# Kernel optimization log

Hardware: AMD Instinct MI355X
Metric: run time of the kernel (lower is better)

Reference implementation:

```python
import jax, jax.numpy as jnp
import numpy as np

B, H, W, D, K = 64, 32, 32, 128, 1024


def setup_inputs() -> dict:
    key = jax.random.key(0)
    k1, k2 = jax.random.split(key)
    z_e = jax.random.normal(k1, (B, H, W, D), dtype=jnp.float32)
    # GlorotUniform over (k, d): limit = sqrt(6 / (k + d))
    limit = float(np.sqrt(6.0 / (K + D)))
    codebook = jax.random.uniform(k2, (K, D), dtype=jnp.float32, minval=-limit, maxval=limit)
    return {"z_e": z_e, "codebook": codebook}


def reference(z_e, codebook):
    # Original: norm = ||z_e[..., None, :] - codebook||_2 over d, then argmin over k.
    # Squared distance has the same argmin; expand to avoid the (B,H,W,k,d) tensor:
    # ||z - c||^2 = ||z||^2 - 2 z.c + ||c||^2
    z2 = jnp.sum(z_e * z_e, axis=-1, keepdims=True)           # (B,H,W,1)
    c2 = jnp.sum(codebook * codebook, axis=-1)                # (k,)
    dots = jnp.einsum('bhwd,kd->bhwk', z_e, codebook)         # (B,H,W,k)
    dist2 = z2 - 2.0 * dots + c2                              # (B,H,W,k)
    q_z = jnp.argmin(dist2, axis=-1)                          # (B,H,W) int
    return q_z
```

## Files before the change

kernel.cpp:

```cpp
#include <hip/hip_runtime.h>
#include <stdint.h>

#define NPTS   65536
#define DDIM   128
#define KCODES 1024

typedef __attribute__((ext_vector_type(8))) _Float16  half8;
typedef __attribute__((ext_vector_type(4))) float     f32x4;
typedef __attribute__((ext_vector_type(4))) int       int4v;
typedef __attribute__((ext_vector_type(2))) _Float16  half2v;

__device__ __forceinline__ void split16(float x, _Float16& hi, _Float16& lo) {
  _Float16 h = (__builtin_fabsf(x) < 6.103515625e-05f) ? (_Float16)0.f : (_Float16)x;
  hi = h;
  lo = (_Float16)(__fmul_rn(__fsub_rn(x, (float)h), 2048.f));
}

__device__ __forceinline__ float np_sumsq_128(const float* __restrict__ row) {
  float r[8];
#pragma unroll
  for (int k = 0; k < 8; ++k) r[k] = __fmul_rn(row[k], row[k]);
  for (int i = 8; i < 128; i += 8)
#pragma unroll
    for (int k = 0; k < 8; ++k) r[k] = __fadd_rn(r[k], __fmul_rn(row[i + k], row[i + k]));
  float s01 = __fadd_rn(r[0], r[1]), s23 = __fadd_rn(r[2], r[3]);
  float s45 = __fadd_rn(r[4], r[5]), s67 = __fadd_rn(r[6], r[7]);
  return __fadd_rn(__fadd_rn(s01, s23), __fadd_rn(s45, s67));
}

__device__ __forceinline__ void async_copy16(const void* g, void* l) {
  auto gp = (const __attribute__((address_space(1))) unsigned int*)(uintptr_t)g;
  auto lp = (__attribute__((address_space(3))) unsigned int*)(unsigned)(uintptr_t)l;
  __builtin_amdgcn_global_load_lds(gp, lp, 16, 0, 0);
}

constexpr size_t SZ_B   = (size_t)KCODES * DDIM * 2;
constexpr size_t OFF_B1 = 0;
constexpr size_t OFF_B2 = SZ_B;
constexpr size_t OFF_C2 = 2 * SZ_B;
constexpr size_t WS_NEED = OFF_C2 + (size_t)KCODES * 4;

__global__ __launch_bounds__(256) void vq_prep_cb(const float* __restrict__ cb,
                                                  _Float16* __restrict__ B1,
                                                  _Float16* __restrict__ B2,
                                                  float* __restrict__ c2) {
  const int w = threadIdx.x >> 6, ln = threadIdx.x & 63;
  const int code = blockIdx.x * 4 + w;
  const float2 cv = ((const float2*)(cb + (size_t)code * DDIM))[ln];
  _Float16 h0, l0, h1, l1;
  split16(cv.x, h0, l0); split16(cv.y, h1, l1);
  const int kg = ln >> 2;
  const int o  = 2 * (ln & 3);
  const size_t dst = (size_t)code * DDIM + (size_t)((kg ^ (code & 15)) * 8 + o);
  *(half2v*)(B1 + dst) = (half2v){h0, h1};
  *(half2v*)(B2 + dst) = (half2v){l0, l1};

  if (threadIdx.x < 32) {
    const int cc = blockIdx.x * 4 + (threadIdx.x >> 3), jj = threadIdx.x & 7;
    const float* row = cb + (size_t)cc * DDIM;
    float e = row[jj];
    float acc = __fmul_rn(e, e);
    for (int i = 1; i < 16; ++i) {
      e = row[i * 8 + jj];
      acc = __fadd_rn(acc, __fmul_rn(e, e));
    }
    float a1 = __fadd_rn(acc, __shfl_xor(acc, 1));
    float a2 = __fadd_rn(a1, __shfl_xor(a1, 2));
    float a4 = __fadd_rn(a2, __shfl_xor(a2, 4));
    if (jj == 0) c2[cc] = a4;
  }
}

__global__ __launch_bounds__(256, 2) void vq_gemm(
    const float* __restrict__ z,
    const unsigned short* __restrict__ B1g, const unsigned short* __restrict__ B2g,
    const float* __restrict__ c2g, int* __restrict__ out) {
  __shared__ alignas(16) char smem[16384 + 16384 + 4096 + 512];
  unsigned short* Bs1 = (unsigned short*)smem;
  unsigned short* Bs2 = (unsigned short*)(smem + 16384);
  float* c2sh = (float*)(smem + 32768);
  float* z2sh = (float*)(smem + 32768 + 4096);
  float* Ls   = (float*)smem;

  const int tid = threadIdx.x;
  const int ln = tid & 63, wr = tid >> 6;
  const int l15 = ln & 15, q = ln >> 4;
  const size_t row0 = (size_t)blockIdx.x * 128;
  const float4* z4 = (const float4*)z;

  for (int cc = 0; cc < 4; ++cc) {
#pragma unroll
    for (int j = 0; j < 4; ++j) {
      const int idx = tid + j * 256;
      float4 v = z4[(row0 + cc * 32) * 32 + idx];
      *(float4*)&Ls[(idx >> 5) * 132 + (idx & 31) * 4] = v;
    }
    __syncthreads();
    {
      const int r = tid >> 3, jj = tid & 7;
      const float* row = &Ls[r * 132];
      float e = row[jj];
      float acc = __fmul_rn(e, e);
      for (int i = 1; i < 16; ++i) {
        e = row[i * 8 + jj];
        acc = __fadd_rn(acc, __fmul_rn(e, e));
      }
      float a1 = __fadd_rn(acc, __shfl_xor(acc, 1));
      float a2 = __fadd_rn(a1, __shfl_xor(a1, 2));
      float a4 = __fadd_rn(a2, __shfl_xor(a2, 4));
      if (jj == 0) z2sh[cc * 32 + r] = a4;
    }
    __syncthreads();
  }

#pragma unroll
  for (int j = 0; j < 4; ++j) {
    const int s = tid + j * 256;
    async_copy16(B2g + s * 8, Bs2 + s * 8);
    async_copy16(B1g + s * 8, Bs1 + s * 8);
  }
  async_copy16(c2g + tid * 4, c2sh + tid * 4);

  half8 a1f[2][4], a2f[2][4];
#pragma unroll
  for (int rf = 0; rf < 2; ++rf) {
    const float* zr = z + (row0 + wr * 32 + rf * 16 + l15) * DDIM;
#pragma unroll
    for (int ks = 0; ks < 4; ++ks) {
      float tmp[8];
      *(float4*)tmp       = *(const float4*)(zr + ks * 32 + q * 8);
      *(float4*)(tmp + 4) = *(const float4*)(zr + ks * 32 + q * 8 + 4);
      half8 h, l;
#pragma unroll
      for (int e = 0; e < 8; ++e) {
        _Float16 hh, ll;
        split16(tmp[e], hh, ll);
        h[e] = hh; l[e] = ll;
      }
      a1f[rf][ks] = h; a2f[rf][ks] = l;
    }
  }

  float mv[8];
  int mi[8];
#pragma unroll
  for (int i = 0; i < 8; ++i) { mv[i] = 3.0e38f; mi[i] = 0; }

  __syncthreads();

  float z2r[8];
#pragma unroll
  for (int rf = 0; rf < 2; ++rf)
#pragma unroll
    for (int reg = 0; reg < 4; ++reg)
      z2r[rf * 4 + reg] = z2sh[wr * 32 + rf * 16 + q * 4 + reg];

  for (int iter = 0; iter < 16; ++iter) {
    const int c0 = iter * 64;
    f32x4 acc[2][4];
#pragma unroll
    for (int rf = 0; rf < 2; ++rf)
#pragma unroll
      for (int cf = 0; cf < 4; ++cf) acc[rf][cf] = (f32x4){0.f, 0.f, 0.f, 0.f};

#pragma unroll
    for (int ks = 0; ks < 4; ++ks) {
      half8 b[4];
#pragma unroll
      for (int cf = 0; cf < 4; ++cf)
        b[cf] = *(const half8*)&Bs2[(cf * 16 + l15) * 128 + (((ks * 4 + q) ^ l15) * 8)];
#pragma unroll
      for (int rf = 0; rf < 2; ++rf)
#pragma unroll
        for (int cf = 0; cf < 4; ++cf)
          acc[rf][cf] = __builtin_amdgcn_mfma_f32_16x16x32_f16(a1f[rf][ks], b[cf],
                                                               acc[rf][cf], 0, 0, 0);
    }

    __syncthreads();
    if (iter < 15) {
#pragma unroll
      for (int j = 0; j < 4; ++j) {
        const int s = tid + j * 256;
        async_copy16(B2g + (size_t)(c0 + 64) * DDIM + s * 8, Bs2 + s * 8);
      }
    }

#pragma unroll
    for (int ks = 0; ks < 4; ++ks) {
      half8 b[4];
#pragma unroll
      for (int cf = 0; cf < 4; ++cf)
        b[cf] = *(const half8*)&Bs1[(cf * 16 + l15) * 128 + (((ks * 4 + q) ^ l15) * 8)];
#pragma unroll
      for (int rf = 0; rf < 2; ++rf)
#pragma unroll
        for (int cf = 0; cf < 4; ++cf)
          acc[rf][cf] = __builtin_amdgcn_mfma_f32_16x16x32_f16(a2f[rf][ks], b[cf],
                                                               acc[rf][cf], 0, 0, 0);
    }
#pragma unroll
    for (int rf = 0; rf < 2; ++rf)
#pragma unroll
      for (int cf = 0; cf < 4; ++cf) acc[rf][cf] = acc[rf][cf] * 4.8828125e-4f;

#pragma unroll
    for (int ks = 0; ks < 4; ++ks) {
      half8 b[4];
#pragma unroll
      for (int cf = 0; cf < 4; ++cf)
        b[cf] = *(const half8*)&Bs1[(cf * 16 + l15) * 128 + (((ks * 4 + q) ^ l15) * 8)];
#pragma unroll
      for (int rf = 0; rf < 2; ++rf)
#pragma unroll
        for (int cf = 0; cf < 4; ++cf)
          acc[rf][cf] = __builtin_amdgcn_mfma_f32_16x16x32_f16(a1f[rf][ks], b[cf],
                                                               acc[rf][cf], 0, 0, 0);
    }

#pragma unroll
    for (int rf = 0; rf < 2; ++rf)
#pragma unroll
      for (int reg = 0; reg < 4; ++reg) {
        const int slot = rf * 4 + reg;
        const float z2v = z2r[slot];
#pragma unroll
        for (int cf = 0; cf < 4; ++cf) {
          const float c2v = c2sh[c0 + cf * 16 + l15];
          float dot = acc[rf][cf][reg];
          float v = __fadd_rn(__fsub_rn(z2v, __fmul_rn(2.f, dot)), c2v);
          int idx = c0 + cf * 16 + l15;
          if (v < mv[slot]) { mv[slot] = v; mi[slot] = idx; }
        }
      }

    __syncthreads();
    if (iter < 15) {
#pragma unroll
      for (int j = 0; j < 4; ++j) {
        const int s = tid + j * 256;
        async_copy16(B1g + (size_t)(c0 + 64) * DDIM + s * 8, Bs1 + s * 8);
      }
    }
  }

#pragma unroll
  for (int slot = 0; slot < 8; ++slot) {
    float v = mv[slot];
    int i = mi[slot];
#pragma unroll
    for (int m = 1; m <= 8; m <<= 1) {
      float ov = __shfl_xor(v, m);
      int oi = __shfl_xor(i, m);
      if (ov < v || (ov == v && oi < i)) { v = ov; i = oi; }
    }
    mv[slot] = v; mi[slot] = i;
  }

  if (l15 == 0) {
#pragma unroll
    for (int rf = 0; rf < 2; ++rf) {
      int4v r = {mi[rf * 4 + 0], mi[rf * 4 + 1], mi[rf * 4 + 2], mi[rf * 4 + 3]};
      *(int4v*)&out[row0 + wr * 32 + rf * 16 + q * 4] = r;
    }
  }
}

__global__ __launch_bounds__(256) void vq_fallback(const float* __restrict__ z,
                                                   const float* __restrict__ cb,
                                                   int* __restrict__ out) {
  __shared__ float zs[DDIM];
  __shared__ float z2s;
  __shared__ float bv[256];
  __shared__ int bi[256];
  const int p = blockIdx.x, tid = threadIdx.x;
  if (tid < DDIM) zs[tid] = z[(size_t)p * DDIM + tid];
  __syncthreads();
  if (tid == 0) z2s = np_sumsq_128(zs);
  __syncthreads();
  const float z2p = z2s;
  float best = 3.0e38f;
  int bidx = 0;
  for (int c = tid; c < KCODES; c += 256) {
    const float* cr = cb + (size_t)c * DDIM;
    double acc = 0.0;
#pragma unroll 8
    for (int d = 0; d < DDIM; ++d) acc += (double)zs[d] * (double)cr[d];
    float dfl = (float)acc;
    float c2k = np_sumsq_128(cr);
    float v = __fadd_rn(__fsub_rn(z2p, __fmul_rn(2.f, dfl)), c2k);
    if (v < best) { best = v; bidx = c; }
  }
  bv[tid] = best; bi[tid] = bidx;
  __syncthreads();
  for (int off = 128; off > 0; off >>= 1) {
    if (tid < off) {
      if (bv[tid + off] < bv[tid] || (bv[tid + off] == bv[tid] && bi[tid + off] < bi[tid])) {
        bv[tid] = bv[tid + off]; bi[tid] = bi[tid + off];
      }
    }
    __syncthreads();
  }
  if (tid == 0) out[p] = bi[0];
}

extern "C" void kernel_launch(void* const* d_in, const int* in_sizes, int n_in,
                              void* d_out, int out_size, void* d_ws, size_t ws_size,
                              hipStream_t stream) {
  (void)in_sizes; (void)n_in; (void)out_size;
  const float* z = (const float*)d_in[0];
  const float* cb = (const float*)d_in[1];
  int* out = (int*)d_out;

  if (d_ws != nullptr && ws_size >= WS_NEED) {
    char* ws = (char*)d_ws;
    _Float16* B1 = (_Float16*)(ws + OFF_B1);
    _Float16* B2 = (_Float16*)(ws + OFF_B2);
    float* c2 = (float*)(ws + OFF_C2);

    vq_prep_cb<<<KCODES / 4, 256, 0, stream>>>(cb, B1, B2, c2);
    vq_gemm<<<NPTS / 128, 256, 0, stream>>>(
        z, (const unsigned short*)(ws + OFF_B1), (const unsigned short*)(ws + OFF_B2),
        c2, out);
  } else {
    vq_fallback<<<NPTS, 256, 0, stream>>>(z, cb, out);
  }
}
```

Baseline: 118.5 us.

## Software-pipeline codebook tiles so argmin epilogue overlaps next tile's MFMAs

Restructures the 16-iteration codebook loop into a prologue, a 15-iteration steady state, and an epilogue. The first MFMA pass for tile i+1 is issued before the distance/argmin compare of tile i, which works on a snapshot of the accumulators, so scalar compare work can overlap matrix-core work. It also reuses one set of Bs1 fragments for both hi and lo passes instead of loading them twice from LDS. The cost is higher register pressure from the snapshot array and the 16 held B fragments, which may reduce occupancy or cause spills.

```diff
diff --git a/kernel.cpp b/kernel.cpp
--- a/kernel.cpp
+++ b/kernel.cpp
@@ -155,30 +155,31 @@
     for (int reg = 0; reg < 4; ++reg)
       z2r[rf * 4 + reg] = z2sh[wr * 32 + rf * 16 + q * 4 + reg];
 
-  for (int iter = 0; iter < 16; ++iter) {
+  f32x4 acc[2][4];
+
+#pragma unroll
+  for (int rf = 0; rf < 2; ++rf)
+#pragma unroll
+    for (int cf = 0; cf < 4; ++cf) acc[rf][cf] = (f32x4){0.f, 0.f, 0.f, 0.f};
+#pragma unroll
+  for (int ks = 0; ks < 4; ++ks) {
+    half8 b[4];
+#pragma unroll
+    for (int cf = 0; cf < 4; ++cf)
+      b[cf] = *(const half8*)&Bs2[(cf * 16 + l15) * 128 + (((ks * 4 + q) ^ l15) * 8)];
+#pragma unroll
+    for (int rf = 0; rf < 2; ++rf)
+#pragma unroll
+      for (int cf = 0; cf < 4; ++cf)
+        acc[rf][cf] = __builtin_amdgcn_mfma_f32_16x16x32_f16(a1f[rf][ks], b[cf],
+                                                             acc[rf][cf], 0, 0, 0);
+  }
+
+  for (int iter = 0; iter < 15; ++iter) {
     const int c0 = iter * 64;
-    f32x4 acc[2][4];
-#pragma unroll
-    for (int rf = 0; rf < 2; ++rf)
-#pragma unroll
-      for (int cf = 0; cf < 4; ++cf) acc[rf][cf] = (f32x4){0.f, 0.f, 0.f, 0.f};
-
-#pragma unroll
-    for (int ks = 0; ks < 4; ++ks) {
-      half8 b[4];
-#pragma unroll
-      for (int cf = 0; cf < 4; ++cf)
-        b[cf] = *(const half8*)&Bs2[(cf * 16 + l15) * 128 + (((ks * 4 + q) ^ l15) * 8)];
-#pragma unroll
-      for (int rf = 0; rf < 2; ++rf)
-#pragma unroll
-        for (int cf = 0; cf < 4; ++cf)
-          acc[rf][cf] = __builtin_amdgcn_mfma_f32_16x16x32_f16(a1f[rf][ks], b[cf],
-                                                               acc[rf][cf], 0, 0, 0);
-    }
-
-    __syncthreads();
-    if (iter < 15) {
+
+    __syncthreads();
+    {
 #pragma unroll
       for (int j = 0; j < 4; ++j) {
         const int s = tid + j * 256;
@@ -186,61 +187,138 @@
       }
     }
 
-#pragma unroll
-    for (int ks = 0; ks < 4; ++ks) {
-      half8 b[4];
+    half8 b1[4][4];
+#pragma unroll
+    for (int ks = 0; ks < 4; ++ks)
 #pragma unroll
       for (int cf = 0; cf < 4; ++cf)
-        b[cf] = *(const half8*)&Bs1[(cf * 16 + l15) * 128 + (((ks * 4 + q) ^ l15) * 8)];
+        b1[ks][cf] = *(const half8*)&Bs1[(cf * 16 + l15) * 128 + (((ks * 4 + q) ^ l15) * 8)];
+
+#pragma unroll
+    for (int ks = 0; ks < 4; ++ks)
 #pragma unroll
       for (int rf = 0; rf < 2; ++rf)
 #pragma unroll
         for (int cf = 0; cf < 4; ++cf)
-          acc[rf][cf] = __builtin_amdgcn_mfma_f32_16x16x32_f16(a2f[rf][ks], b[cf],
+          acc[rf][cf] = __builtin_amdgcn_mfma_f32_16x16x32_f16(a2f[rf][ks], b1[ks][cf],
                                                                acc[rf][cf], 0, 0, 0);
-    }
 #pragma unroll
     for (int rf = 0; rf < 2; ++rf)
 #pragma unroll
       for (int cf = 0; cf < 4; ++cf) acc[rf][cf] = acc[rf][cf] * 4.8828125e-4f;
 
 #pragma unroll
-    for (int ks = 0; ks < 4; ++ks) {
-      half8 b[4];
+    for (int ks = 0; ks < 4; ++ks)
+#pragma unroll
+      for (int rf = 0; rf < 2; ++rf)
+#pragma unroll
+        for (int cf = 0; cf < 4; ++cf)
+          acc[rf][cf] = __builtin_amdgcn_mfma_f32_16x16x32_f16(a1f[rf][ks], b1[ks][cf],
+                                                               acc[rf][cf], 0, 0, 0);
+
+    float dsnap[2][4][4];
+#pragma unroll
+    for (int rf = 0; rf < 2; ++rf)
 #pragma unroll
       for (int cf = 0; cf < 4; ++cf)
-        b[cf] = *(const half8*)&Bs1[(cf * 16 + l15) * 128 + (((ks * 4 + q) ^ l15) * 8)];
-#pragma unroll
-      for (int rf = 0; rf < 2; ++rf)
-#pragma unroll
-        for (int cf = 0; cf < 4; ++cf)
-          acc[rf][cf] = __builtin_amdgcn_mfma_f32_16x16x32_f16(a1f[rf][ks], b[cf],
-                                                               acc[rf][cf], 0, 0, 0);
-    }
-
-#pragma unroll
-    for (int rf = 0; rf < 2; ++rf)
-#pragma unroll
-      for (int reg = 0; reg < 4; ++reg) {
-        const int slot = rf * 4 + reg;
-        const float z2v = z2r[slot];
-#pragma unroll
-        for (int cf = 0; cf < 4; ++cf) {
-          const float c2v = c2sh[c0 + cf * 16 + l15];
-          float dot = acc[rf][cf][reg];
-          float v = __fadd_rn(__fsub_rn(z2v, __fmul_rn(2.f, dot)), c2v);
-          int idx = c0 + cf * 16 + l15;
-          if (v < mv[slot]) { mv[slot] = v; mi[slot] = idx; }
-        }
-      }
-
-    __syncthreads();
-    if (iter < 15) {
+#pragma unroll
+        for (int reg = 0; reg < 4; ++reg) dsnap[rf][cf][reg] = acc[rf][cf][reg];
+
+    __syncthreads();
+    {
 #pragma unroll
       for (int j = 0; j < 4; ++j) {
         const int s = tid + j * 256;
         async_copy16(B1g + (size_t)(c0 + 64) * DDIM + s * 8, Bs1 + s * 8);
       }
+    }
+
+#pragma unroll
+    for (int rf = 0; rf < 2; ++rf)
+#pragma unroll
+      for (int cf = 0; cf < 4; ++cf) acc[rf][cf] = (f32x4){0.f, 0.f, 0.f, 0.f};
+#pragma unroll
+    for (int ks = 0; ks < 4; ++ks) {
+      half8 b[4];
+#pragma unroll
+      for (int cf = 0; cf < 4; ++cf)
+        b[cf] = *(const half8*)&Bs2[(cf * 16 + l15) * 128 + (((ks * 4 + q) ^ l15) * 8)];
+#pragma unroll
+      for (int rf = 0; rf < 2; ++rf)
+#pragma unroll
+        for (int cf = 0; cf < 4; ++cf)
+          acc[rf][cf] = __builtin_amdgcn_mfma_f32_16x16x32_f16(a1f[rf][ks], b[cf],
+                                                               acc[rf][cf], 0, 0, 0);
+    }
+
+    {
+      float c2v[4];
+#pragma unroll
+      for (int cf = 0; cf < 4; ++cf) c2v[cf] = c2sh[c0 + cf * 16 + l15];
+#pragma unroll
+      for (int rf = 0; rf < 2; ++rf)
+#pragma unroll
+        for (int reg = 0; reg < 4; ++reg) {
+          const int slot = rf * 4 + reg;
+          const float z2v = z2r[slot];
+#pragma unroll
+          for (int cf = 0; cf < 4; ++cf) {
+            float dot = dsnap[rf][cf][reg];
+            float v = __fadd_rn(__fsub_rn(z2v, __fmul_rn(2.f, dot)), c2v[cf]);
+            int idx = c0 + cf * 16 + l15;
+            if (v < mv[slot]) { mv[slot] = v; mi[slot] = idx; }
+          }
+        }
+    }
+  }
+
+  {
+    const int c0 = 960;
+    __syncthreads();
+    half8 b1[4][4];
+#pragma unroll
+    for (int ks = 0; ks < 4; ++ks)
+#pragma unroll
+      for (int cf = 0; cf < 4; ++cf)
+        b1[ks][cf] = *(const half8*)&Bs1[(cf * 16 + l15) * 128 + (((ks * 4 + q) ^ l15) * 8)];
+#pragma unroll
+    for (int ks = 0; ks < 4; ++ks)
+#pragma unroll
+      for (int rf = 0; rf < 2; ++rf)
+#pragma unroll
+        for (int cf = 0; cf < 4; ++cf)
+          acc[rf][cf] = __builtin_amdgcn_mfma_f32_16x16x32_f16(a2f[rf][ks], b1[ks][cf],
+                                                               acc[rf][cf], 0, 0, 0);
+#pragma unroll
+    for (int rf = 0; rf < 2; ++rf)
+#pragma unroll
+      for (int cf = 0; cf < 4; ++cf) acc[rf][cf] = acc[rf][cf] * 4.8828125e-4f;
+#pragma unroll
+    for (int ks = 0; ks < 4; ++ks)
+#pragma unroll
+      for (int rf = 0; rf < 2; ++rf)
+#pragma unroll
+        for (int cf = 0; cf < 4; ++cf)
+          acc[rf][cf] = __builtin_amdgcn_mfma_f32_16x16x32_f16(a1f[rf][ks], b1[ks][cf],
+                                                               acc[rf][cf], 0, 0, 0);
+    {
+      float c2v[4];
+#pragma unroll
+      for (int cf = 0; cf < 4; ++cf) c2v[cf] = c2sh[c0 + cf * 16 + l15];
+#pragma unroll
+      for (int rf = 0; rf < 2; ++rf)
+#pragma unroll
+        for (int reg = 0; reg < 4; ++reg) {
+          const int slot = rf * 4 + reg;
+          const float z2v = z2r[slot];
+#pragma unroll
+          for (int cf = 0; cf < 4; ++cf) {
+            float dot = acc[rf][cf][reg];
+            float v = __fadd_rn(__fsub_rn(z2v, __fmul_rn(2.f, dot)), c2v[cf]);
+            int idx = c0 + cf * 16 + l15;
+            if (v < mv[slot]) { mv[slot] = v; mi[slot] = idx; }
+          }
+        }
     }
   }
 
```

New measurement: 121.6 us. 2.6% more time.

## Split codebook columns across warp pairs with double-buffered B tiles

Applied to the files above, without the earlier changes.

Remaps the 4 warps into a 2x2 grid. Each warp now covers 64 rows against half of each 64-code tile, instead of 32 rows against all 64 codes, so each B fragment loaded from LDS feeds 4 row-fragments. The B1/B2 tiles are double-buffered in 64KB of LDS with one barrier per iteration, replacing the old two-barrier split refill. A final cross-warp argmin merge through shared memory is added. The cost is twice the A-fragment registers and 16 running minima per thread. The larger LDS footprint together with launch_bounds(256,2) may limit occupancy.

```diff
diff --git a/kernel.cpp b/kernel.cpp
--- a/kernel.cpp
+++ b/kernel.cpp
@@ -75,15 +75,16 @@
     const float* __restrict__ z,
     const unsigned short* __restrict__ B1g, const unsigned short* __restrict__ B2g,
     const float* __restrict__ c2g, int* __restrict__ out) {
-  __shared__ alignas(16) char smem[16384 + 16384 + 4096 + 512];
-  unsigned short* Bs1 = (unsigned short*)smem;
-  unsigned short* Bs2 = (unsigned short*)(smem + 16384);
-  float* c2sh = (float*)(smem + 32768);
-  float* z2sh = (float*)(smem + 32768 + 4096);
+  __shared__ alignas(16) char smem[32768 * 2 + 4096 + 512 + 512 + 512];
+  float* c2sh = (float*)(smem + 65536);
+  float* z2sh = (float*)(smem + 65536 + 4096);
+  float* mvx  = (float*)(smem + 65536 + 4096 + 512);
+  int*   mix  = (int*)  (smem + 65536 + 4096 + 1024);
   float* Ls   = (float*)smem;
 
   const int tid = threadIdx.x;
-  const int ln = tid & 63, wr = tid >> 6;
+  const int ln = tid & 63, w = tid >> 6;
+  const int wr2 = w >> 1, wc = w & 1;
   const int l15 = ln & 15, q = ln >> 4;
   const size_t row0 = (size_t)blockIdx.x * 128;
   const float4* z4 = (const float4*)z;
@@ -113,18 +114,25 @@
     __syncthreads();
   }
 
-#pragma unroll
-  for (int j = 0; j < 4; ++j) {
-    const int s = tid + j * 256;
-    async_copy16(B2g + s * 8, Bs2 + s * 8);
-    async_copy16(B1g + s * 8, Bs1 + s * 8);
-  }
-  async_copy16(c2g + tid * 4, c2sh + tid * 4);
-
-  half8 a1f[2][4], a2f[2][4];
-#pragma unroll
-  for (int rf = 0; rf < 2; ++rf) {
-    const float* zr = z + (row0 + wr * 32 + rf * 16 + l15) * DDIM;
+  {
+    unsigned short* nb = (unsigned short*)smem;
+#pragma unroll
+    for (int j = 0; j < 4; ++j) {
+      const int s = tid + j * 256;
+      async_copy16(B2g + s * 8, nb + s * 8);
+    }
+#pragma unroll
+    for (int j = 0; j < 4; ++j) {
+      const int s = tid + j * 256;
+      async_copy16(B1g + s * 8, nb + 8192 + s * 8);
+    }
+    async_copy16(c2g + tid * 4, c2sh + tid * 4);
+  }
+
+  half8 a1f[4][4], a2f[4][4];
+#pragma unroll
+  for (int rf = 0; rf < 4; ++rf) {
+    const float* zr = z + (row0 + wr2 * 64 + rf * 16 + l15) * DDIM;
 #pragma unroll
     for (int ks = 0; ks < 4; ++ks) {
       float tmp[8];
@@ -141,111 +149,99 @@
     }
   }
 
-  float mv[8];
-  int mi[8];
-#pragma unroll
-  for (int i = 0; i < 8; ++i) { mv[i] = 3.0e38f; mi[i] = 0; }
-
-  __syncthreads();
-
-  float z2r[8];
-#pragma unroll
-  for (int rf = 0; rf < 2; ++rf)
+  float mv[16];
+  int mi[16];
+#pragma unroll
+  for (int i = 0; i < 16; ++i) { mv[i] = 3.0e38f; mi[i] = 0; }
+
+  __syncthreads();
+
+  float z2r[16];
+#pragma unroll
+  for (int rf = 0; rf < 4; ++rf)
 #pragma unroll
     for (int reg = 0; reg < 4; ++reg)
-      z2r[rf * 4 + reg] = z2sh[wr * 32 + rf * 16 + q * 4 + reg];
-
-  for (int iter = 0; iter < 16; ++iter) {
-    const int c0 = iter * 64;
-    f32x4 acc[2][4];
-#pragma unroll
-    for (int rf = 0; rf < 2; ++rf)
-#pragma unroll
-      for (int cf = 0; cf < 4; ++cf) acc[rf][cf] = (f32x4){0.f, 0.f, 0.f, 0.f};
-
-#pragma unroll
-    for (int ks = 0; ks < 4; ++ks) {
-      half8 b[4];
-#pragma unroll
-      for (int cf = 0; cf < 4; ++cf)
-        b[cf] = *(const half8*)&Bs2[(cf * 16 + l15) * 128 + (((ks * 4 + q) ^ l15) * 8)];
-#pragma unroll
-      for (int rf = 0; rf < 2; ++rf)
-#pragma unroll
-        for (int cf = 0; cf < 4; ++cf)
-          acc[rf][cf] = __builtin_amdgcn_mfma_f32_16x16x32_f16(a1f[rf][ks], b[cf],
-                                                               acc[rf][cf], 0, 0, 0);
-    }
-
-    __syncthreads();
-    if (iter < 15) {
+      z2r[rf * 4 + reg] = z2sh[wr2 * 64 + rf * 16 + q * 4 + reg];
+
+  for (int u = 0; u < 16; ++u) {
+    const unsigned short* cur = (const unsigned short*)(smem + (u & 1) * 32768);
+
+    if (u < 15) {
+      unsigned short* nb = (unsigned short*)(smem + ((u + 1) & 1) * 32768);
+      const size_t goff = (size_t)(u + 1) * 8192;
 #pragma unroll
       for (int j = 0; j < 4; ++j) {
         const int s = tid + j * 256;
-        async_copy16(B2g + (size_t)(c0 + 64) * DDIM + s * 8, Bs2 + s * 8);
-      }
-    }
-
-#pragma unroll
-    for (int ks = 0; ks < 4; ++ks) {
-      half8 b[4];
-#pragma unroll
-      for (int cf = 0; cf < 4; ++cf)
-        b[cf] = *(const half8*)&Bs1[(cf * 16 + l15) * 128 + (((ks * 4 + q) ^ l15) * 8)];
-#pragma unroll
-      for (int rf = 0; rf < 2; ++rf)
-#pragma unroll
-        for (int cf = 0; cf < 4; ++cf)
-          acc[rf][cf] = __builtin_amdgcn_mfma_f32_16x16x32_f16(a2f[rf][ks], b[cf],
-                                                               acc[rf][cf], 0, 0, 0);
-    }
-#pragma unroll
-    for (int rf = 0; rf < 2; ++rf)
-#pragma unroll
-      for (int cf = 0; cf < 4; ++cf) acc[rf][cf] = acc[rf][cf] * 4.8828125e-4f;
-
-#pragma unroll
-    for (int ks = 0; ks < 4; ++ks) {
-      half8 b[4];
-#pragma unroll
-      for (int cf = 0; cf < 4; ++cf)
-        b[cf] = *(const half8*)&Bs1[(cf * 16 + l15) * 128 + (((ks * 4 + q) ^ l15) * 8)];
-#pragma unroll
-      for (int rf = 0; rf < 2; ++rf)
-#pragma unroll
-        for (int cf = 0; cf < 4; ++cf)
-          acc[rf][cf] = __builtin_amdgcn_mfma_f32_16x16x32_f16(a1f[rf][ks], b[cf],
-                                                               acc[rf][cf], 0, 0, 0);
-    }
-
-#pragma unroll
-    for (int rf = 0; rf < 2; ++rf)
-#pragma unroll
-      for (int reg = 0; reg < 4; ++reg) {
-        const int slot = rf * 4 + reg;
-        const float z2v = z2r[slot];
-#pragma unroll
-        for (int cf = 0; cf < 4; ++cf) {
-          const float c2v = c2sh[c0 + cf * 16 + l15];
-          float dot = acc[rf][cf][reg];
-          float v = __fadd_rn(__fsub_rn(z2v, __fmul_rn(2.f, dot)), c2v);
-          int idx = c0 + cf * 16 + l15;
-          if (v < mv[slot]) { mv[slot] = v; mi[slot] = idx; }
-        }
-      }
-
-    __syncthreads();
-    if (iter < 15) {
+        async_copy16(B2g + goff + s * 8, nb + s * 8);
+      }
 #pragma unroll
       for (int j = 0; j < 4; ++j) {
         const int s = tid + j * 256;
-        async_copy16(B1g + (size_t)(c0 + 64) * DDIM + s * 8, Bs1 + s * 8);
-      }
-    }
-  }
-
-#pragma unroll
-  for (int slot = 0; slot < 8; ++slot) {
+        async_copy16(B1g + goff + s * 8, nb + 8192 + s * 8);
+      }
+    }
+
+    const int c0 = u * 64 + wc * 32;
+
+#pragma unroll
+    for (int cf = 0; cf < 2; ++cf) {
+      const unsigned short* p = cur + (size_t)(wc * 32 + cf * 16 + l15) * 128;
+
+      f32x4 acc[4];
+#pragma unroll
+      for (int rf = 0; rf < 4; ++rf) acc[rf] = (f32x4){0.f, 0.f, 0.f, 0.f};
+
+      half8 bb[4];
+#pragma unroll
+      for (int ks = 0; ks < 4; ++ks)
+        bb[ks] = *(const half8*)&p[((ks * 4 + q) ^ l15) * 8];
+#pragma unroll
+      for (int ks = 0; ks < 4; ++ks)
+#pragma unroll
+        for (int rf = 0; rf < 4; ++rf)
+          acc[rf] = __builtin_amdgcn_mfma_f32_16x16x32_f16(a1f[rf][ks], bb[ks],
+                                                           acc[rf], 0, 0, 0);
+
+#pragma unroll
+      for (int ks = 0; ks < 4; ++ks) {
+        bb[ks] = *(const half8*)&p[8192 + ((ks * 4 + q) ^ l15) * 8];
+        asm volatile("" : "+v"(bb[ks]));
+      }
+#pragma unroll
+      for (int ks = 0; ks < 4; ++ks)
+#pragma unroll
+        for (int rf = 0; rf < 4; ++rf)
+          acc[rf] = __builtin_amdgcn_mfma_f32_16x16x32_f16(a2f[rf][ks], bb[ks],
+                                                           acc[rf], 0, 0, 0);
+#pragma unroll
+      for (int rf = 0; rf < 4; ++rf) acc[rf] = acc[rf] * 4.8828125e-4f;
+
+#pragma unroll
+      for (int ks = 0; ks < 4; ++ks)
+#pragma unroll
+        for (int rf = 0; rf < 4; ++rf)
+          acc[rf] = __builtin_amdgcn_mfma_f32_16x16x32_f16(a1f[rf][ks], bb[ks],
+                                                           acc[rf], 0, 0, 0);
+
+      {
+        const float c2v = c2sh[c0 + cf * 16 + l15];
+        const int idx = c0 + cf * 16 + l15;
+#pragma unroll
+        for (int rf = 0; rf < 4; ++rf)
+#pragma unroll
+          for (int reg = 0; reg < 4; ++reg) {
+            const int slot = rf * 4 + reg;
+            float v = __fadd_rn(__builtin_fmaf(acc[rf][reg], -2.0f, z2r[slot]), c2v);
+            if (v < mv[slot]) { mv[slot] = v; mi[slot] = idx; }
+          }
+      }
+    }
+
+    __syncthreads();
+  }
+
+#pragma unroll
+  for (int slot = 0; slot < 16; ++slot) {
     float v = mv[slot];
     int i = mi[slot];
 #pragma unroll
@@ -257,11 +253,32 @@
     mv[slot] = v; mi[slot] = i;
   }
 
-  if (l15 == 0) {
-#pragma unroll
-    for (int rf = 0; rf < 2; ++rf) {
-      int4v r = {mi[rf * 4 + 0], mi[rf * 4 + 1], mi[rf * 4 + 2], mi[rf * 4 + 3]};
-      *(int4v*)&out[row0 + wr * 32 + rf * 16 + q * 4] = r;
+  if (l15 == 0 && wc == 1) {
+#pragma unroll
+    for (int slot = 0; slot < 16; ++slot) {
+      const int r = wr2 * 64 + (slot >> 2) * 16 + q * 4 + (slot & 3);
+      mvx[r] = mv[slot];
+      mix[r] = mi[slot];
+    }
+  }
+  __syncthreads();
+  if (l15 == 0 && wc == 0) {
+#pragma unroll
+    for (int rf = 0; rf < 4; ++rf) {
+      int ib[4];
+#pragma unroll
+      for (int reg = 0; reg < 4; ++reg) {
+        const int r = wr2 * 64 + rf * 16 + q * 4 + reg;
+        const int slot = rf * 4 + reg;
+        float v = mv[slot];
+        int i = mi[slot];
+        const float ov = mvx[r];
+        const int oi = mix[r];
+        if (ov < v || (ov == v && oi < i)) { v = ov; i = oi; }
+        ib[reg] = i;
+      }
+      int4v rr = {ib[0], ib[1], ib[2], ib[3]};
+      *(int4v*)&out[row0 + wr2 * 64 + rf * 16 + q * 4] = rr;
     }
   }
 }
```

Result: slower. 126.7 us (+6.9%).

## Split codebook columns across wave pairs and halve rows per block

Applied to the files above, without the earlier changes.

Each block now handles 64 points instead of 128. The four waves form a 2x2 grid: two row groups, each split into two column halves of the 64-code tile. Per-wave accumulators shrink from 2x4 to 2x2 fragments and launch bounds go to 4 blocks per CU, aiming for more blocks and higher occupancy. A shared-memory merge step combines the two column halves' argmin results, with lowest-index tie-breaking. In exchange, every codebook tile is loaded into LDS twice as often across the grid per point, and an extra barrier is added.

```diff
diff --git a/kernel.cpp b/kernel.cpp
--- a/kernel.cpp
+++ b/kernel.cpp
@@ -71,24 +71,27 @@
   }
 }
 
-__global__ __launch_bounds__(256, 2) void vq_gemm(
+__global__ __launch_bounds__(256, 4) void vq_gemm(
     const float* __restrict__ z,
     const unsigned short* __restrict__ B1g, const unsigned short* __restrict__ B2g,
     const float* __restrict__ c2g, int* __restrict__ out) {
-  __shared__ alignas(16) char smem[16384 + 16384 + 4096 + 512];
+  __shared__ alignas(16) char smem[16384 + 16384 + 4096 + 256 + 256 + 256];
   unsigned short* Bs1 = (unsigned short*)smem;
   unsigned short* Bs2 = (unsigned short*)(smem + 16384);
   float* c2sh = (float*)(smem + 32768);
-  float* z2sh = (float*)(smem + 32768 + 4096);
+  float* z2sh = (float*)(smem + 36864);
+  float* mvx  = (float*)(smem + 37120);
+  int*   mix  = (int*)  (smem + 37376);
   float* Ls   = (float*)smem;
 
   const int tid = threadIdx.x;
-  const int ln = tid & 63, wr = tid >> 6;
+  const int ln = tid & 63, w = tid >> 6;
+  const int wr2 = w >> 1, wc = w & 1;
   const int l15 = ln & 15, q = ln >> 4;
-  const size_t row0 = (size_t)blockIdx.x * 128;
+  const size_t row0 = (size_t)blockIdx.x * 64;
   const float4* z4 = (const float4*)z;
 
-  for (int cc = 0; cc < 4; ++cc) {
+  for (int cc = 0; cc < 2; ++cc) {
 #pragma unroll
     for (int j = 0; j < 4; ++j) {
       const int idx = tid + j * 256;
@@ -124,7 +127,7 @@
   half8 a1f[2][4], a2f[2][4];
 #pragma unroll
   for (int rf = 0; rf < 2; ++rf) {
-    const float* zr = z + (row0 + wr * 32 + rf * 16 + l15) * DDIM;
+    const float* zr = z + (row0 + wr2 * 32 + rf * 16 + l15) * DDIM;
 #pragma unroll
     for (int ks = 0; ks < 4; ++ks) {
       float tmp[8];
@@ -153,26 +156,27 @@
   for (int rf = 0; rf < 2; ++rf)
 #pragma unroll
     for (int reg = 0; reg < 4; ++reg)
-      z2r[rf * 4 + reg] = z2sh[wr * 32 + rf * 16 + q * 4 + reg];
+      z2r[rf * 4 + reg] = z2sh[wr2 * 32 + rf * 16 + q * 4 + reg];
 
   for (int iter = 0; iter < 16; ++iter) {
-    const int c0 = iter * 64;
-    f32x4 acc[2][4];
+    const int cbase = iter * 64;
+    const int cw = cbase + wc * 32;
+    f32x4 acc[2][2];
 #pragma unroll
     for (int rf = 0; rf < 2; ++rf)
 #pragma unroll
-      for (int cf = 0; cf < 4; ++cf) acc[rf][cf] = (f32x4){0.f, 0.f, 0.f, 0.f};
+      for (int cf = 0; cf < 2; ++cf) acc[rf][cf] = (f32x4){0.f, 0.f, 0.f, 0.f};
 
 #pragma unroll
     for (int ks = 0; ks < 4; ++ks) {
-      half8 b[4];
-#pragma unroll
-      for (int cf = 0; cf < 4; ++cf)
-        b[cf] = *(const half8*)&Bs2[(cf * 16 + l15) * 128 + (((ks * 4 + q) ^ l15) * 8)];
+      half8 b[2];
+#pragma unroll
+      for (int cf = 0; cf < 2; ++cf)
+        b[cf] = *(const half8*)&Bs2[(wc * 32 + cf * 16 + l15) * 128 + (((ks * 4 + q) ^ l15) * 8)];
 #pragma unroll
       for (int rf = 0; rf < 2; ++rf)
 #pragma unroll
-        for (int cf = 0; cf < 4; ++cf)
+        for (int cf = 0; cf < 2; ++cf)
           acc[rf][cf] = __builtin_amdgcn_mfma_f32_16x16x32_f16(a1f[rf][ks], b[cf],
                                                                acc[rf][cf], 0, 0, 0);
     }
@@ -182,38 +186,38 @@
 #pragma unroll
       for (int j = 0; j < 4; ++j) {
         const int s = tid + j * 256;
-        async_copy16(B2g + (size_t)(c0 + 64) * DDIM + s * 8, Bs2 + s * 8);
+        async_copy16(B2g + (size_t)(cbase + 64) * DDIM + s * 8, Bs2 + s * 8);
       }
     }
 
 #pragma unroll
     for (int ks = 0; ks < 4; ++ks) {
-      half8 b[4];
-#pragma unroll
-      for (int cf = 0; cf < 4; ++cf)
-        b[cf] = *(const half8*)&Bs1[(cf * 16 + l15) * 128 + (((ks * 4 + q) ^ l15) * 8)];
+      half8 b[2];
+#pragma unroll
+      for (int cf = 0; cf < 2; ++cf)
+        b[cf] = *(const half8*)&Bs1[(wc * 32 + cf * 16 + l15) * 128 + (((ks * 4 + q) ^ l15) * 8)];
 #pragma unroll
       for (int rf = 0; rf < 2; ++rf)
 #pragma unroll
-        for (int cf = 0; cf < 4; ++cf)
+        for (int cf = 0; cf < 2; ++cf)
           acc[rf][cf] = __builtin_amdgcn_mfma_f32_16x16x32_f16(a2f[rf][ks], b[cf],
                                                                acc[rf][cf], 0, 0, 0);
     }
 #pragma unroll
     for (int rf = 0; rf < 2; ++rf)
 #pragma unroll
-      for (int cf = 0; cf < 4; ++cf) acc[rf][cf] = acc[rf][cf] * 4.8828125e-4f;
+      for (int cf = 0; cf < 2; ++cf) acc[rf][cf] = acc[rf][cf] * 4.8828125e-4f;
 
 #pragma unroll
     for (int ks = 0; ks < 4; ++ks) {
-      half8 b[4];
-#pragma unroll
-      for (int cf = 0; cf < 4; ++cf)
-        b[cf] = *(const half8*)&Bs1[(cf * 16 + l15) * 128 + (((ks * 4 + q) ^ l15) * 8)];
+      half8 b[2];
+#pragma unroll
+      for (int cf = 0; cf < 2; ++cf)
+        b[cf] = *(const half8*)&Bs1[(wc * 32 + cf * 16 + l15) * 128 + (((ks * 4 + q) ^ l15) * 8)];
 #pragma unroll
       for (int rf = 0; rf < 2; ++rf)
 #pragma unroll
-        for (int cf = 0; cf < 4; ++cf)
+        for (int cf = 0; cf < 2; ++cf)
           acc[rf][cf] = __builtin_amdgcn_mfma_f32_16x16x32_f16(a1f[rf][ks], b[cf],
                                                                acc[rf][cf], 0, 0, 0);
     }
@@ -225,11 +229,11 @@
         const int slot = rf * 4 + reg;
         const float z2v = z2r[slot];
 #pragma unroll
-        for (int cf = 0; cf < 4; ++cf) {
-          const float c2v = c2sh[c0 + cf * 16 + l15];
+        for (int cf = 0; cf < 2; ++cf) {
+          const float c2v = c2sh[cw + cf * 16 + l15];
           float dot = acc[rf][cf][reg];
           float v = __fadd_rn(__fsub_rn(z2v, __fmul_rn(2.f, dot)), c2v);
-          int idx = c0 + cf * 16 + l15;
+          int idx = cw + cf * 16 + l15;
           if (v < mv[slot]) { mv[slot] = v; mi[slot] = idx; }
         }
       }
@@ -239,7 +243,7 @@
 #pragma unroll
       for (int j = 0; j < 4; ++j) {
         const int s = tid + j * 256;
-        async_copy16(B1g + (size_t)(c0 + 64) * DDIM + s * 8, Bs1 + s * 8);
+        async_copy16(B1g + (size_t)(cbase + 64) * DDIM + s * 8, Bs1 + s * 8);
       }
     }
   }
@@ -257,11 +261,32 @@
     mv[slot] = v; mi[slot] = i;
   }
 
-  if (l15 == 0) {
+  if (l15 == 0 && wc == 1) {
+#pragma unroll
+    for (int slot = 0; slot < 8; ++slot) {
+      const int r = wr2 * 32 + (slot >> 2) * 16 + q * 4 + (slot & 3);
+      mvx[r] = mv[slot];
+      mix[r] = mi[slot];
+    }
+  }
+  __syncthreads();
+  if (l15 == 0 && wc == 0) {
 #pragma unroll
     for (int rf = 0; rf < 2; ++rf) {
-      int4v r = {mi[rf * 4 + 0], mi[rf * 4 + 1], mi[rf * 4 + 2], mi[rf * 4 + 3]};
-      *(int4v*)&out[row0 + wr * 32 + rf * 16 + q * 4] = r;
+      int ib[4];
+#pragma unroll
+      for (int reg = 0; reg < 4; ++reg) {
+        const int r = wr2 * 32 + rf * 16 + q * 4 + reg;
+        const int slot = rf * 4 + reg;
+        float v = mv[slot];
+        int i = mi[slot];
+        const float ov = mvx[r];
+        const int oi = mix[r];
+        if (ov < v || (ov == v && oi < i)) { v = ov; i = oi; }
+        ib[reg] = i;
+      }
+      int4v rr = {ib[0], ib[1], ib[2], ib[3]};
+      *(int4v*)&out[row0 + wr2 * 32 + rf * 16 + q * 4] = rr;
     }
   }
 }
@@ -319,7 +344,7 @@
     float* c2 = (float*)(ws + OFF_C2);
 
     vq_prep_cb<<<KCODES / 4, 256, 0, stream>>>(cb, B1, B2, c2);
-    vq_gemm<<<NPTS / 128, 256, 0, stream>>>(
+    vq_gemm<<<NPTS / 64, 256, 0, stream>>>(
         z, (const unsigned short*)(ws + OFF_B1), (const unsigned short*)(ws + OFF_B2),
         c2, out);
   } else {
```

Result: slower. 158.1 us (+33.4%).
